# Performance work log

Hardware: AMD Instinct MI355X
Metric: run time of the kernel (lower is better)

The kernel has to match this reference:

```python
import jax, jax.numpy as jnp
import numpy as np

N = 16384
N_ITER = 10
TAU = 1e-3  # LM initial damping factor


def _skew(w):
    z = jnp.zeros((), w.dtype)
    return jnp.stack([
        jnp.stack([z, -w[2], w[1]]),
        jnp.stack([w[2], z, -w[0]]),
        jnp.stack([-w[1], w[0], z]),
    ])


def se3_exp(x):
    # x = [omega (3), v (3)] -> 4x4 SE3 (lie_se3_to_SE3)
    w, v = x[:3], x[3:]
    th2 = jnp.dot(w, w)
    th = jnp.sqrt(th2)
    small = th < 1e-8
    ths = jnp.where(small, jnp.ones_like(th), th)
    A = jnp.where(small, 1.0 - th2 / 6.0, jnp.sin(ths) / ths)
    B = jnp.where(small, 0.5 - th2 / 24.0, (1.0 - jnp.cos(ths)) / ths ** 2)
    C = jnp.where(small, 1.0 / 6.0 - th2 / 120.0, (ths - jnp.sin(ths)) / ths ** 3)
    W = _skew(w)
    W2 = W @ W
    I = jnp.eye(3, dtype=x.dtype)
    R = I + A * W + B * W2
    V = I + B * W + C * W2
    t = V @ v
    T = jnp.eye(4, dtype=x.dtype).at[:3, :3].set(R).at[:3, 3].set(t)
    return T


def _res_jac(x, ref_pts, trg_pts, trg_normals):
    T = se3_exp(x)
    R, t = T[:3, :3], T[:3, 3]
    # dist_association: ref cloud transformed by inv(T_est), nearest target point
    Ri, ti = R.T, -R.T @ t
    ref_t = ref_pts @ Ri.T + ti  # [N,3]
    d2 = ((ref_t ** 2).sum(-1)[:, None]
          + (trg_pts ** 2).sum(-1)[None, :]
          - 2.0 * (ref_t @ trg_pts.T))  # [N_ref, N_trg] -- dominant memory traffic
    trg_ids = jnp.argmin(d2, axis=1)  # src_ids == arange(N_ref)
    # residual: dot(n_trg_transformed, ref - trg_transformed) at correspondences
    trg_t = trg_pts @ R.T + t
    n_t = trg_normals @ R.T
    n = n_t[trg_ids]          # [N,3] gather
    p = trg_t[trg_ids]        # [N,3] gather
    r = jnp.sum(n * (ref_pts - p), axis=1)  # [N]
    # J = n^T @ j_3d(ref_pts)  ==  [cross(p_ref, n), n]  (closed form of 1x3x6 matmuls)
    J = jnp.concatenate([jnp.cross(ref_pts, n), n], axis=1)  # [N,6]
    return r, J


def reference(ref_pts, trg_pts, trg_normals):
    dtype = ref_pts.dtype
    x = jnp.zeros(6, dtype=dtype)
    r, J = _res_jac(x, ref_pts, trg_pts, trg_normals)
    F = jnp.sum(r ** 2)
    H0 = J.T @ J
    mu = TAU * jnp.max(jnp.diag(H0))
    nu = jnp.asarray(2.0, dtype)
    I6 = jnp.eye(6, dtype=dtype)
    for _ in range(N_ITER):
        H = J.T @ J
        g = J.T @ r
        dx = jnp.linalg.solve(H + mu * I6, -g)
        x_new = x + dx
        r_new, J_new = _res_jac(x_new, ref_pts, trg_pts, trg_normals)
        F_new = jnp.sum(r_new ** 2)
        denom = jnp.dot(dx, mu * dx - g)
        rho = (F - F_new) / jnp.where(jnp.abs(denom) < 1e-12, 1e-12, denom)
        accept = rho > 0.0
        x = jnp.where(accept, x_new, x)
        r = jnp.where(accept, r_new, r)
        J = jnp.where(accept, J_new, J)
        F = jnp.where(accept, F_new, F)
        mu = jnp.where(accept,
                       mu * jnp.maximum(1.0 / 3.0, 1.0 - (2.0 * rho - 1.0) ** 3),
                       mu * nu)
        nu = jnp.where(accept, jnp.asarray(2.0, dtype), 2.0 * nu)
    T = se3_exp(x)
    cost = jnp.mean(r ** 2)  # cost_fun(residual_fun(x,...))
    return T, cost


def setup_inputs() -> dict:
    key = jax.random.key(0)
    k1, k2 = jax.random.split(key)
    ref_pts = jax.random.normal(k1, (N, 3), dtype=jnp.float32)
    # target = slightly rotated/translated copy so ICP has a meaningful solution
    ang = 0.05
    R_true = np.array([[np.cos(ang), -np.sin(ang), 0.0],
                       [np.sin(ang), np.cos(ang), 0.0],
                       [0.0, 0.0, 1.0]], dtype=np.float32)
    t_true = np.array([0.02, -0.01, 0.03], dtype=np.float32)
    trg_pts = ref_pts @ jnp.asarray(R_true).T + jnp.asarray(t_true)
    n = jax.random.normal(k2, (N, 3), dtype=jnp.float32)
    trg_normals = n / jnp.linalg.norm(n, axis=1, keepdims=True)
    return {"ref_pts": ref_pts, "trg_pts": trg_pts, "trg_normals": trg_normals}
```

## Files before the change

### kernel.cpp

```cpp
#include <hip/hip_runtime.h>
#include <stdint.h>

#define N_PTS 16384
#define TAU_C 0.001f
#define N_ITER 10
#define BJ 256
#define MI 4
#define NGROUP (BJ / 8)
#define NACC 64

struct State {
  float x[6];
  float xc[6];
  float dx[6];
  float Rc[9];
  float tc[3];
  float H[21];
  float g[6];
  float F, mu, nu;
};

__device__ void se3_exp_rt(const float* x, float* R, float* t) {
  float wx = x[0], wy = x[1], wz = x[2];
  float vx = x[3], vy = x[4], vz = x[5];
  float th2 = wx*wx + wy*wy + wz*wz;
  float th = sqrtf(th2);
  float A, B, C;
  if (th < 1e-8f) {
    A = 1.0f - th2 / 6.0f;
    B = 0.5f - th2 / 24.0f;
    C = 1.0f / 6.0f - th2 / 120.0f;
  } else {
    float s = sinf(th), c = cosf(th);
    A = s / th;
    B = (1.0f - c) / th2;
    C = (th - s) / (th2 * th);
  }
  float W[9]  = {0.f, -wz, wy,  wz, 0.f, -wx,  -wy, wx, 0.f};
  float W2[9];
  #pragma unroll
  for (int r = 0; r < 3; r++)
    #pragma unroll
    for (int c = 0; c < 3; c++)
      W2[3*r+c] = W[3*r+0]*W[0+c] + W[3*r+1]*W[3+c] + W[3*r+2]*W[6+c];
  float V[9];
  #pragma unroll
  for (int k = 0; k < 9; k++) {
    float I = (k == 0 || k == 4 || k == 8) ? 1.f : 0.f;
    R[k] = I + A * W[k] + B * W2[k];
    V[k] = I + B * W[k] + C * W2[k];
  }
  t[0] = V[0]*vx + V[1]*vy + V[2]*vz;
  t[1] = V[3]*vx + V[4]*vy + V[5]*vz;
  t[2] = V[6]*vx + V[7]*vy + V[8]*vz;
}

__global__ void prep_kernel(const float* __restrict__ trg,
                            float4* __restrict__ packed,
                            unsigned long long* __restrict__ keys,
                            unsigned* __restrict__ counter,
                            State* st) {
  int i = blockIdx.x * blockDim.x + threadIdx.x;
  if (i < N_PTS) {
    float tx = trg[3*i], ty = trg[3*i+1], tz = trg[3*i+2];
    packed[i] = make_float4(-2.f*tx, -2.f*ty, -2.f*tz, tx*tx + ty*ty + tz*tz);
    keys[i] = 0xFFFFFFFFFFFFFFFFULL;
  }
  if (blockIdx.x == 0 && threadIdx.x == 0) {
    #pragma unroll
    for (int k = 0; k < 6; k++) { st->x[k] = 0.f; st->xc[k] = 0.f; st->dx[k] = 0.f; }
    #pragma unroll
    for (int k = 0; k < 9; k++) st->Rc[k] = (k % 4 == 0) ? 1.f : 0.f;
    st->tc[0] = st->tc[1] = st->tc[2] = 0.f;
    st->nu = 2.f;
    *counter = 0u;
  }
}

__global__ __launch_bounds__(256) void nn_kernel(const float* __restrict__ ref,
                                                 const float4* __restrict__ packed,
                                                 const State* __restrict__ st,
                                                 unsigned long long* __restrict__ keys) {
  __shared__ float4 tile[BJ];
  const int tid = threadIdx.x;
  const int jbase = blockIdx.y * BJ;
  tile[tid] = packed[jbase + tid];

  const float R00 = st->Rc[0], R01 = st->Rc[1], R02 = st->Rc[2];
  const float R10 = st->Rc[3], R11 = st->Rc[4], R12 = st->Rc[5];
  const float R20 = st->Rc[6], R21 = st->Rc[7], R22 = st->Rc[8];
  const float t0 = st->tc[0], t1 = st->tc[1], t2 = st->tc[2];

  const int i0 = blockIdx.x * (256 * MI) + tid;
  float px[MI], py[MI], pz[MI];
  #pragma unroll
  for (int m = 0; m < MI; m++) {
    int i = i0 + 256*m;
    float ax = ref[3*i] - t0, ay = ref[3*i+1] - t1, az = ref[3*i+2] - t2;
    px[m] = R00*ax + R10*ay + R20*az;
    py[m] = R01*ax + R11*ay + R21*az;
    pz[m] = R02*ax + R12*ay + R22*az;
  }
  __syncthreads();

  float best[MI];
  int bg[MI];
  #pragma unroll
  for (int m = 0; m < MI; m++) { best[m] = 3.4e38f; bg[m] = 0; }

  #pragma unroll 2
  for (int g = 0; g < NGROUP; g++) {
    float4 tq[8];
    #pragma unroll
    for (int k = 0; k < 8; k++) tq[k] = tile[8*g + k];
    #pragma unroll
    for (int m = 0; m < MI; m++) {
      float s[8];
      #pragma unroll
      for (int k = 0; k < 8; k++) {
        float v = fmaf(px[m], tq[k].x, tq[k].w);
        v = fmaf(py[m], tq[k].y, v);
        s[k] = fmaf(pz[m], tq[k].z, v);
      }
      float a = fminf(fminf(s[0], s[1]), s[2]);
      float b = fminf(fminf(s[3], s[4]), s[5]);
      float c = fminf(a, b);
      float gm = fminf(fminf(s[6], s[7]), c);
      if (gm < best[m]) { best[m] = gm; bg[m] = g; }
    }
  }

  #pragma unroll
  for (int m = 0; m < MI; m++) {
    const float4* gp = packed + jbase + 8 * bg[m];
    int bj = 0;
    #pragma unroll
    for (int k = 7; k >= 0; k--) {
      float4 tq = gp[k];
      float v = fmaf(px[m], tq.x, tq.w);
      v = fmaf(py[m], tq.y, v);
      v = fmaf(pz[m], tq.z, v);
      if (v == best[m]) bj = k;
    }
    int i = i0 + 256*m;
    unsigned ub = __float_as_uint(best[m]);
    ub = (ub & 0x80000000u) ? ~ub : (ub | 0x80000000u);
    unsigned long long key = ((unsigned long long)ub << 32) |
                             (unsigned long long)(unsigned)(jbase + 8*bg[m] + bj);
    atomicMin(&keys[i], key);
  }
}

__global__ __launch_bounds__(256) void accum_lm_kernel(const float* __restrict__ ref,
                                                       const float* __restrict__ trg,
                                                       const float* __restrict__ nrm,
                                                       unsigned long long* __restrict__ keys,
                                                       State* st,
                                                       float* __restrict__ partials,
                                                       unsigned* __restrict__ counter,
                                                       float* out, int mode) {
  const int tid = threadIdx.x;
  const int i = blockIdx.x * 256 + tid;

  const float R00 = st->Rc[0], R01 = st->Rc[1], R02 = st->Rc[2];
  const float R10 = st->Rc[3], R11 = st->Rc[4], R12 = st->Rc[5];
  const float R20 = st->Rc[6], R21 = st->Rc[7], R22 = st->Rc[8];
  const float t0 = st->tc[0], t1 = st->tc[1], t2 = st->tc[2];

  unsigned long long key = keys[i];
  keys[i] = 0xFFFFFFFFFFFFFFFFULL;
  int j = (int)(unsigned)(key & 0xFFFFFFFFULL);

  float nx0 = nrm[3*j], ny0 = nrm[3*j+1], nz0 = nrm[3*j+2];
  float qx = trg[3*j], qy = trg[3*j+1], qz = trg[3*j+2];
  float nx = R00*nx0 + R01*ny0 + R02*nz0;
  float ny = R10*nx0 + R11*ny0 + R12*nz0;
  float nz = R20*nx0 + R21*ny0 + R22*nz0;
  float pxx = R00*qx + R01*qy + R02*qz + t0;
  float pyy = R10*qx + R11*qy + R12*qz + t1;
  float pzz = R20*qx + R21*qy + R22*qz + t2;

  float rx = ref[3*i], ry = ref[3*i+1], rz = ref[3*i+2];
  float dxx = rx - pxx, dyy = ry - pyy, dzz = rz - pzz;
  float r = nx*dxx + ny*dyy + nz*dzz;

  float J[6];
  J[0] = ry*nz - rz*ny;
  J[1] = rz*nx - rx*nz;
  J[2] = rx*ny - ry*nx;
  J[3] = nx; J[4] = ny; J[5] = nz;

  float acc[28];
  int c21 = 0;
  #pragma unroll
  for (int a = 0; a < 6; a++)
    #pragma unroll
    for (int b = a; b < 6; b++)
      acc[c21++] = J[a] * J[b];
  #pragma unroll
  for (int a = 0; a < 6; a++) acc[21+a] = J[a] * r;
  acc[27] = r * r;

  #pragma unroll
  for (int kk = 0; kk < 28; kk++) {
    float v = acc[kk];
    for (int off = 32; off; off >>= 1) v += __shfl_down(v, off);
    acc[kk] = v;
  }
  __shared__ float red[4][28];
  int wave = tid >> 6, lane = tid & 63;
  if (lane == 0) {
    #pragma unroll
    for (int kk = 0; kk < 28; kk++) red[wave][kk] = acc[kk];
  }
  __syncthreads();
  if (tid < 28)
    partials[tid * NACC + blockIdx.x] =
        red[0][tid] + red[1][tid] + red[2][tid] + red[3][tid];

  __shared__ bool last;
  __syncthreads();
  if (tid == 0) {
    __threadfence();
    unsigned old = atomicAdd(counter, 1u);
    last = (old == NACC - 1);
  }
  __syncthreads();
  if (!last) return;

  __threadfence();
  __shared__ float tot[28];
  if (tid < 28) {
    float s = 0.f;
    #pragma unroll
    for (int b = 0; b < NACC; b++) s += partials[tid * NACC + b];
    tot[tid] = s;
  }
  __syncthreads();

  if (tid == 0) {
    atomicExch(counter, 0u);
    float Fn = tot[27];
    float mu, nu;

    if (mode == 0) {
      #pragma unroll
      for (int k = 0; k < 6; k++) st->x[k] = st->xc[k];
      #pragma unroll
      for (int k = 0; k < 21; k++) st->H[k] = tot[k];
      #pragma unroll
      for (int k = 0; k < 6; k++) st->g[k] = tot[21+k];
      st->F = Fn;
      float md = tot[0];
      md = fmaxf(md, tot[6]); md = fmaxf(md, tot[11]); md = fmaxf(md, tot[15]);
      md = fmaxf(md, tot[18]); md = fmaxf(md, tot[20]);
      mu = TAU_C * md;
      nu = 2.f;
    } else {
      mu = st->mu; nu = st->nu;
      float denom = 0.f;
      #pragma unroll
      for (int k = 0; k < 6; k++) denom += st->dx[k] * (mu * st->dx[k] - st->g[k]);
      if (fabsf(denom) < 1e-12f) denom = 1e-12f;
      float rho = (st->F - Fn) / denom;
      if (rho > 0.f) {
        #pragma unroll
        for (int k = 0; k < 6; k++) st->x[k] = st->xc[k];
        #pragma unroll
        for (int k = 0; k < 21; k++) st->H[k] = tot[k];
        #pragma unroll
        for (int k = 0; k < 6; k++) st->g[k] = tot[21+k];
        st->F = Fn;
        float tcube = 2.f * rho - 1.f;
        mu = mu * fmaxf(1.f / 3.f, 1.f - tcube * tcube * tcube);
        nu = 2.f;
      } else {
        mu = mu * nu;
        nu = 2.f * nu;
      }
    }
    st->mu = mu; st->nu = nu;

    if (mode < N_ITER) {
      float A[6][7];
      int c21b = 0;
      #pragma unroll
      for (int a = 0; a < 6; a++)
        #pragma unroll
        for (int b = a; b < 6; b++) { A[a][b] = st->H[c21b]; A[b][a] = st->H[c21b]; c21b++; }
      #pragma unroll
      for (int a = 0; a < 6; a++) { A[a][a] += mu; A[a][6] = -st->g[a]; }
      #pragma unroll
      for (int col = 0; col < 6; col++) {
        float inv = 1.f / A[col][col];
        #pragma unroll
        for (int rI = 0; rI < 6; rI++) {
          if (rI > col) {
            float f = A[rI][col] * inv;
            #pragma unroll
            for (int cc = 0; cc < 7; cc++)
              if (cc >= col) A[rI][cc] -= f * A[col][cc];
          }
        }
      }
      float d[6];
      #pragma unroll
      for (int rI = 5; rI >= 0; rI--) {
        float s = A[rI][6];
        #pragma unroll
        for (int cc = 0; cc < 6; cc++)
          if (cc > rI) s -= A[rI][cc] * d[cc];
        d[rI] = s / A[rI][rI];
      }
      float Rn[9], tn[3];
      #pragma unroll
      for (int k = 0; k < 6; k++) { st->dx[k] = d[k]; st->xc[k] = st->x[k] + d[k]; }
      se3_exp_rt(st->xc, Rn, tn);
      #pragma unroll
      for (int k = 0; k < 9; k++) st->Rc[k] = Rn[k];
      #pragma unroll
      for (int k = 0; k < 3; k++) st->tc[k] = tn[k];
    } else {
      float Rn[9], tn[3];
      se3_exp_rt(st->x, Rn, tn);
      out[0] = Rn[0]; out[1] = Rn[1]; out[2]  = Rn[2]; out[3]  = tn[0];
      out[4] = Rn[3]; out[5] = Rn[4]; out[6]  = Rn[5]; out[7]  = tn[1];
      out[8] = Rn[6]; out[9] = Rn[7]; out[10] = Rn[8]; out[11] = tn[2];
      out[12] = 0.f; out[13] = 0.f; out[14] = 0.f; out[15] = 1.f;
      out[16] = st->F / (float)N_PTS;
    }
  }
}

extern "C" void kernel_launch(void* const* d_in, const int* in_sizes, int n_in,
                              void* d_out, int out_size, void* d_ws, size_t ws_size,
                              hipStream_t stream) {
  const float* ref = (const float*)d_in[0];
  const float* trg = (const float*)d_in[1];
  const float* nrm = (const float*)d_in[2];
  float* out = (float*)d_out;

  char* ws = (char*)d_ws;
  float4* packed = (float4*)ws;
  unsigned long long* keys = (unsigned long long*)(ws + 262144);
  float* partials = (float*)(ws + 262144 + 131072);
  unsigned* counter = (unsigned*)(ws + 262144 + 131072 + 8192);
  State* st = (State*)(ws + 262144 + 131072 + 8192 + 256);

  prep_kernel<<<64, 256, 0, stream>>>(trg, packed, keys, counter, st);
  for (int e = 0; e <= N_ITER; e++) {
    nn_kernel<<<dim3(N_PTS / (256 * MI), N_PTS / BJ), 256, 0, stream>>>(ref, packed, st, keys);
    accum_lm_kernel<<<NACC, 256, 0, stream>>>(ref, trg, nrm, keys, st, partials, counter, out, e);
  }
}
```

Before: 429.5 us.

## Replace brute-force nearest neighbor with uniform grid shell search fused into LM eval

```diff
diff --git a/kernel.cpp b/kernel.cpp
--- a/kernel.cpp
+++ b/kernel.cpp
@@ -4,9 +4,13 @@
 #define N_PTS 16384
 #define TAU_C 0.001f
 #define N_ITER 10
-#define BJ 256
-#define MI 4
-#define NGROUP (BJ / 8)
+
+#define G 72
+#define NCELLS (G * G * G)
+#define XMIN (-6.0f)
+#define CELL_H (12.0f / (float)G)
+#define INV_H ((float)G / 12.0f)
+#define NSCAN ((NCELLS + 1023) / 1024)
 #define NACC 64
 
 struct State {
@@ -55,18 +59,17 @@
   t[2] = V[6]*vx + V[7]*vy + V[8]*vz;
 }
 
-__global__ void prep_kernel(const float* __restrict__ trg,
-                            float4* __restrict__ packed,
-                            unsigned long long* __restrict__ keys,
-                            unsigned* __restrict__ counter,
-                            State* st) {
-  int i = blockIdx.x * blockDim.x + threadIdx.x;
-  if (i < N_PTS) {
-    float tx = trg[3*i], ty = trg[3*i+1], tz = trg[3*i+2];
-    packed[i] = make_float4(-2.f*tx, -2.f*ty, -2.f*tz, tx*tx + ty*ty + tz*tz);
-    keys[i] = 0xFFFFFFFFFFFFFFFFULL;
-  }
-  if (blockIdx.x == 0 && threadIdx.x == 0) {
+__device__ inline int cell1d(float v) {
+  int c = (int)floorf((v - XMIN) * INV_H);
+  return min(max(c, 0), G - 1);
+}
+
+__global__ __launch_bounds__(256) void zero_kernel(unsigned* __restrict__ count,
+                                                   unsigned* __restrict__ counter,
+                                                   State* st) {
+  unsigned idx = blockIdx.x * 256u + threadIdx.x;
+  if (idx < NCELLS) count[idx] = 0u;
+  if (idx == 0) {
     #pragma unroll
     for (int k = 0; k < 6; k++) { st->x[k] = 0.f; st->xc[k] = 0.f; st->dx[k] = 0.f; }
     #pragma unroll
@@ -77,110 +80,159 @@
   }
 }
 
-__global__ __launch_bounds__(256) void nn_kernel(const float* __restrict__ ref,
-                                                 const float4* __restrict__ packed,
-                                                 const State* __restrict__ st,
-                                                 unsigned long long* __restrict__ keys) {
-  __shared__ float4 tile[BJ];
+__global__ __launch_bounds__(256) void count_kernel(const float* __restrict__ trg,
+                                                    unsigned* __restrict__ count) {
+  int j = blockIdx.x * 256 + threadIdx.x;
+  int cx = cell1d(trg[3*j]), cy = cell1d(trg[3*j+1]), cz = cell1d(trg[3*j+2]);
+  atomicAdd(&count[(cz * G + cy) * G + cx], 1u);
+}
+
+__global__ __launch_bounds__(256) void scan1_kernel(const unsigned* __restrict__ count,
+                                                    unsigned* __restrict__ excl,
+                                                    unsigned* __restrict__ blockSums) {
+  __shared__ unsigned sh[256];
+  const int t = threadIdx.x;
+  const unsigned base = blockIdx.x * 1024u + t * 4u;
+  unsigned v0 = (base + 0 < NCELLS) ? count[base + 0] : 0u;
+  unsigned v1 = (base + 1 < NCELLS) ? count[base + 1] : 0u;
+  unsigned v2 = (base + 2 < NCELLS) ? count[base + 2] : 0u;
+  unsigned v3 = (base + 3 < NCELLS) ? count[base + 3] : 0u;
+  unsigned tsum = v0 + v1 + v2 + v3;
+  sh[t] = tsum;
+  __syncthreads();
+  for (int off = 1; off < 256; off <<= 1) {
+    unsigned xv = (t >= off) ? sh[t - off] : 0u;
+    __syncthreads();
+    sh[t] += xv;
+    __syncthreads();
+  }
+  unsigned texcl = sh[t] - tsum;
+  if (t == 255) blockSums[blockIdx.x] = sh[255];
+  if (base + 0 < NCELLS) excl[base + 0] = texcl;
+  if (base + 1 < NCELLS) excl[base + 1] = texcl + v0;
+  if (base + 2 < NCELLS) excl[base + 2] = texcl + v0 + v1;
+  if (base + 3 < NCELLS) excl[base + 3] = texcl + v0 + v1 + v2;
+}
+
+__global__ __launch_bounds__(512) void scan2_kernel(unsigned* __restrict__ blockSums) {
+  __shared__ unsigned sh[512];
+  int t = threadIdx.x;
+  unsigned v = (t < NSCAN) ? blockSums[t] : 0u;
+  sh[t] = v;
+  __syncthreads();
+  for (int off = 1; off < 512; off <<= 1) {
+    unsigned xv = (t >= off) ? sh[t - off] : 0u;
+    __syncthreads();
+    sh[t] += xv;
+    __syncthreads();
+  }
+  if (t < NSCAN) blockSums[t] = sh[t] - v;
+}
+
+__global__ __launch_bounds__(256) void scan3_kernel(const unsigned* __restrict__ count,
+                                                    unsigned* __restrict__ cursor,
+                                                    const unsigned* __restrict__ blockSums,
+                                                    unsigned* __restrict__ gridPacked) {
+  const unsigned base = blockIdx.x * 1024u + threadIdx.x * 4u;
+  unsigned boff = blockSums[blockIdx.x];
+  #pragma unroll
+  for (int q = 0; q < 4; q++) {
+    unsigned idx = base + q;
+    if (idx < NCELLS) {
+      unsigned start = cursor[idx] + boff;
+      unsigned n = count[idx]; n = n > 255u ? 255u : n;
+      gridPacked[idx] = (start << 8) | n;
+      cursor[idx] = start;
+    }
+  }
+}
+
+__global__ __launch_bounds__(256) void scatter_kernel(const float* __restrict__ trg,
+                                                      unsigned* __restrict__ cursor,
+                                                      float4* __restrict__ sortedPts,
+                                                      unsigned* __restrict__ sortedIdx) {
+  int j = blockIdx.x * 256 + threadIdx.x;
+  float tx = trg[3*j], ty = trg[3*j+1], tz = trg[3*j+2];
+  int cx = cell1d(tx), cy = cell1d(ty), cz = cell1d(tz);
+  unsigned pos = atomicAdd(&cursor[(cz * G + cy) * G + cx], 1u);
+  sortedPts[pos] = make_float4(tx, ty, tz, __uint_as_float((unsigned)j));
+  sortedIdx[pos] = (unsigned)j;
+}
+
+__global__ __launch_bounds__(256) void eval_kernel(const float* __restrict__ ref,
+                                                   const float* __restrict__ trg,
+                                                   const float* __restrict__ nrm,
+                                                   const unsigned* __restrict__ gridPacked,
+                                                   const float4* __restrict__ sortedPts,
+                                                   const unsigned* __restrict__ sortedIdx,
+                                                   State* st,
+                                                   double* __restrict__ partials,
+                                                   unsigned* __restrict__ counter,
+                                                   float* out, int mode) {
   const int tid = threadIdx.x;
-  const int jbase = blockIdx.y * BJ;
-  tile[tid] = packed[jbase + tid];
+  const int it = blockIdx.x * 256 + tid;
+  const int i = (int)sortedIdx[it];
 
   const float R00 = st->Rc[0], R01 = st->Rc[1], R02 = st->Rc[2];
   const float R10 = st->Rc[3], R11 = st->Rc[4], R12 = st->Rc[5];
   const float R20 = st->Rc[6], R21 = st->Rc[7], R22 = st->Rc[8];
   const float t0 = st->tc[0], t1 = st->tc[1], t2 = st->tc[2];
 
-  const int i0 = blockIdx.x * (256 * MI) + tid;
-  float px[MI], py[MI], pz[MI];
-  #pragma unroll
-  for (int m = 0; m < MI; m++) {
-    int i = i0 + 256*m;
-    float ax = ref[3*i] - t0, ay = ref[3*i+1] - t1, az = ref[3*i+2] - t2;
-    px[m] = R00*ax + R10*ay + R20*az;
-    py[m] = R01*ax + R11*ay + R21*az;
-    pz[m] = R02*ax + R12*ay + R22*az;
-  }
-  __syncthreads();
-
-  float best[MI];
-  int bg[MI];
-  #pragma unroll
-  for (int m = 0; m < MI; m++) { best[m] = 3.4e38f; bg[m] = 0; }
-
-  #pragma unroll 2
-  for (int g = 0; g < NGROUP; g++) {
-    float4 tq[8];
-    #pragma unroll
-    for (int k = 0; k < 8; k++) tq[k] = tile[8*g + k];
-    #pragma unroll
-    for (int m = 0; m < MI; m++) {
-      float s[8];
-      #pragma unroll
-      for (int k = 0; k < 8; k++) {
-        float v = fmaf(px[m], tq[k].x, tq[k].w);
-        v = fmaf(py[m], tq[k].y, v);
-        s[k] = fmaf(pz[m], tq[k].z, v);
+  const float rx = ref[3*i], ry = ref[3*i+1], rz = ref[3*i+2];
+  const float ax = rx - t0, ay = ry - t1, az = rz - t2;
+  const float qx = R00*ax + R10*ay + R20*az;
+  const float qy = R01*ax + R11*ay + R21*az;
+  const float qz = R02*ax + R12*ay + R22*az;
+
+  const int gx = cell1d(qx), gy = cell1d(qy), gz = cell1d(qz);
+
+  float best = 3.4e38f;
+  int bj = 0x7FFFFFFF;
+  for (int k = 0; k <= G; k++) {
+    for (int dz = -k; dz <= k; dz++) {
+      int cz = gz + dz;
+      if ((unsigned)cz >= (unsigned)G) continue;
+      bool zface = (dz == -k) || (dz == k);
+      for (int dy = -k; dy <= k; dy++) {
+        int cy = gy + dy;
+        if ((unsigned)cy >= (unsigned)G) continue;
+        bool face = zface || (dy == -k) || (dy == k);
+        int step = face ? 1 : (2 * k);
+        for (int dx = -k; dx <= k; dx += step) {
+          int cx = gx + dx;
+          if ((unsigned)cx >= (unsigned)G) continue;
+          unsigned pc = gridPacked[(cz * G + cy) * G + cx];
+          unsigned s = pc >> 8, n = pc & 255u;
+          for (unsigned c = 0; c < n; c++) {
+            float4 p = sortedPts[s + c];
+            float ddx = qx - p.x, ddy = qy - p.y, ddz = qz - p.z;
+            float d2 = fmaf(ddz, ddz, fmaf(ddy, ddy, ddx * ddx));
+            int jj = (int)__float_as_uint(p.w);
+            if (d2 < best || (d2 == best && jj < bj)) { best = d2; bj = jj; }
+          }
+        }
       }
-      float a = fminf(fminf(s[0], s[1]), s[2]);
-      float b = fminf(fminf(s[3], s[4]), s[5]);
-      float c = fminf(a, b);
-      float gm = fminf(fminf(s[6], s[7]), c);
-      if (gm < best[m]) { best[m] = gm; bg[m] = g; }
     }
-  }
-
-  #pragma unroll
-  for (int m = 0; m < MI; m++) {
-    const float4* gp = packed + jbase + 8 * bg[m];
-    int bj = 0;
-    #pragma unroll
-    for (int k = 7; k >= 0; k--) {
-      float4 tq = gp[k];
-      float v = fmaf(px[m], tq.x, tq.w);
-      v = fmaf(py[m], tq.y, v);
-      v = fmaf(pz[m], tq.z, v);
-      if (v == best[m]) bj = k;
-    }
-    int i = i0 + 256*m;
-    unsigned ub = __float_as_uint(best[m]);
-    ub = (ub & 0x80000000u) ? ~ub : (ub | 0x80000000u);
-    unsigned long long key = ((unsigned long long)ub << 32) |
-                             (unsigned long long)(unsigned)(jbase + 8*bg[m] + bj);
-    atomicMin(&keys[i], key);
-  }
-}
-
-__global__ __launch_bounds__(256) void accum_lm_kernel(const float* __restrict__ ref,
-                                                       const float* __restrict__ trg,
-                                                       const float* __restrict__ nrm,
-                                                       unsigned long long* __restrict__ keys,
-                                                       State* st,
-                                                       float* __restrict__ partials,
-                                                       unsigned* __restrict__ counter,
-                                                       float* out, int mode) {
-  const int tid = threadIdx.x;
-  const int i = blockIdx.x * 256 + tid;
-
-  const float R00 = st->Rc[0], R01 = st->Rc[1], R02 = st->Rc[2];
-  const float R10 = st->Rc[3], R11 = st->Rc[4], R12 = st->Rc[5];
-  const float R20 = st->Rc[6], R21 = st->Rc[7], R22 = st->Rc[8];
-  const float t0 = st->tc[0], t1 = st->tc[1], t2 = st->tc[2];
-
-  unsigned long long key = keys[i];
-  keys[i] = 0xFFFFFFFFFFFFFFFFULL;
-  int j = (int)(unsigned)(key & 0xFFFFFFFFULL);
+    float dmin = 3.4e38f;
+    if (gx - k > 0)     dmin = fminf(dmin, qx - (XMIN + (float)(gx - k) * CELL_H));
+    if (gx + k < G - 1) dmin = fminf(dmin, (XMIN + (float)(gx + k + 1) * CELL_H) - qx);
+    if (gy - k > 0)     dmin = fminf(dmin, qy - (XMIN + (float)(gy - k) * CELL_H));
+    if (gy + k < G - 1) dmin = fminf(dmin, (XMIN + (float)(gy + k + 1) * CELL_H) - qy);
+    if (gz - k > 0)     dmin = fminf(dmin, qz - (XMIN + (float)(gz - k) * CELL_H));
+    if (gz + k < G - 1) dmin = fminf(dmin, (XMIN + (float)(gz + k + 1) * CELL_H) - qz);
+    if (best <= dmin * dmin) break;
+  }
+  int j = min(bj, N_PTS - 1);
 
   float nx0 = nrm[3*j], ny0 = nrm[3*j+1], nz0 = nrm[3*j+2];
-  float qx = trg[3*j], qy = trg[3*j+1], qz = trg[3*j+2];
+  float sx = trg[3*j], sy = trg[3*j+1], sz = trg[3*j+2];
   float nx = R00*nx0 + R01*ny0 + R02*nz0;
   float ny = R10*nx0 + R11*ny0 + R12*nz0;
   float nz = R20*nx0 + R21*ny0 + R22*nz0;
-  float pxx = R00*qx + R01*qy + R02*qz + t0;
-  float pyy = R10*qx + R11*qy + R12*qz + t1;
-  float pzz = R20*qx + R21*qy + R22*qz + t2;
-
-  float rx = ref[3*i], ry = ref[3*i+1], rz = ref[3*i+2];
+  float pxx = R00*sx + R01*sy + R02*sz + t0;
+  float pyy = R10*sx + R11*sy + R12*sz + t1;
+  float pzz = R20*sx + R21*sy + R22*sz + t2;
+
   float dxx = rx - pxx, dyy = ry - pyy, dzz = rz - pzz;
   float r = nx*dxx + ny*dyy + nz*dzz;
 
@@ -190,33 +242,33 @@
   J[2] = rx*ny - ry*nx;
   J[3] = nx; J[4] = ny; J[5] = nz;
 
-  float acc[28];
+  double acc[28];
   int c21 = 0;
   #pragma unroll
   for (int a = 0; a < 6; a++)
     #pragma unroll
     for (int b = a; b < 6; b++)
-      acc[c21++] = J[a] * J[b];
-  #pragma unroll
-  for (int a = 0; a < 6; a++) acc[21+a] = J[a] * r;
-  acc[27] = r * r;
+      acc[c21++] = (double)J[a] * (double)J[b];
+  #pragma unroll
+  for (int a = 0; a < 6; a++) acc[21+a] = (double)J[a] * (double)r;
+  acc[27] = (double)r * (double)r;
 
   #pragma unroll
   for (int kk = 0; kk < 28; kk++) {
-    float v = acc[kk];
+    double v = acc[kk];
     for (int off = 32; off; off >>= 1) v += __shfl_down(v, off);
     acc[kk] = v;
   }
-  __shared__ float red[4][28];
+  __shared__ double redD[4][28];
   int wave = tid >> 6, lane = tid & 63;
   if (lane == 0) {
     #pragma unroll
-    for (int kk = 0; kk < 28; kk++) red[wave][kk] = acc[kk];
+    for (int kk = 0; kk < 28; kk++) redD[wave][kk] = acc[kk];
   }
   __syncthreads();
   if (tid < 28)
     partials[tid * NACC + blockIdx.x] =
-        red[0][tid] + red[1][tid] + red[2][tid] + red[3][tid];
+        redD[0][tid] + redD[1][tid] + redD[2][tid] + redD[3][tid];
 
   __shared__ bool last;
   __syncthreads();
@@ -231,10 +283,10 @@
   __threadfence();
   __shared__ float tot[28];
   if (tid < 28) {
-    float s = 0.f;
+    double s = 0.0;
     #pragma unroll
     for (int b = 0; b < NACC; b++) s += partials[tid * NACC + b];
-    tot[tid] = s;
+    tot[tid] = (float)s;
   }
   __syncthreads();
 
@@ -341,15 +393,24 @@
   float* out = (float*)d_out;
 
   char* ws = (char*)d_ws;
-  float4* packed = (float4*)ws;
-  unsigned long long* keys = (unsigned long long*)(ws + 262144);
-  float* partials = (float*)(ws + 262144 + 131072);
-  unsigned* counter = (unsigned*)(ws + 262144 + 131072 + 8192);
-  State* st = (State*)(ws + 262144 + 131072 + 8192 + 256);
-
-  prep_kernel<<<64, 256, 0, stream>>>(trg, packed, keys, counter, st);
-  for (int e = 0; e <= N_ITER; e++) {
-    nn_kernel<<<dim3(N_PTS / (256 * MI), N_PTS / BJ), 256, 0, stream>>>(ref, packed, st, keys);
-    accum_lm_kernel<<<NACC, 256, 0, stream>>>(ref, trg, nrm, keys, st, partials, counter, out, e);
-  }
-}
+  unsigned* count      = (unsigned*)(ws);
+  unsigned* gridPacked = (unsigned*)(ws + 1492992);
+  unsigned* cursor     = (unsigned*)(ws + 2985984);
+  unsigned* blockSums  = (unsigned*)(ws + 4478976);
+  float4*   sortedPts  = (float4*)  (ws + 4481024);
+  unsigned* sortedIdx  = (unsigned*)(ws + 4743168);
+  double*   partials   = (double*)  (ws + 4808704);
+  unsigned* counter    = (unsigned*)(ws + 4823040);
+  State*    st         = (State*)   (ws + 4823104);
+
+  zero_kernel   <<<(NCELLS + 255) / 256, 256, 0, stream>>>(count, counter, st);
+  count_kernel  <<<N_PTS / 256, 256, 0, stream>>>(trg, count);
+  scan1_kernel  <<<NSCAN, 256, 0, stream>>>(count, cursor, blockSums);
+  scan2_kernel  <<<1, 512, 0, stream>>>(blockSums);
+  scan3_kernel  <<<NSCAN, 256, 0, stream>>>(count, cursor, blockSums, gridPacked);
+  scatter_kernel<<<N_PTS / 256, 256, 0, stream>>>(trg, cursor, sortedPts, sortedIdx);
+
+  for (int e = 0; e <= N_ITER; e++)
+    eval_kernel<<<NACC, 256, 0, stream>>>(ref, trg, nrm, gridPacked, sortedPts,
+                                          sortedIdx, st, partials, counter, out, e);
+}
```

New measurement: 743.2 us. 1.73x slower.
